# Kernel optimization log

Measured on AMD Instinct MI355X. Metric: run time of the kernel, lower is better.

## Reference

```python
import jax, jax.numpy as jnp
import numpy as np

D_MODEL = 1024
N_HEADS = 16
D_HEAD = 64
LAMBDA_INIT = 0.8  # paper: 0.8 - 0.6*exp(-0.3*(layer-1)); layer=1 -> 0.8


def setup_inputs() -> dict:
    key = jax.random.key(0)
    ks = jax.random.split(key, 6)
    B, S = 2, 2048
    std = 0.02
    x = jax.random.normal(ks[0], (B, S, D_MODEL), dtype=jnp.float32)
    Wq = jax.random.normal(ks[1], (D_MODEL, 2 * N_HEADS * D_HEAD), dtype=jnp.float32) * std
    Wk = jax.random.normal(ks[2], (D_MODEL, 2 * N_HEADS * D_HEAD), dtype=jnp.float32) * std
    Wv = jax.random.normal(ks[3], (D_MODEL, 2 * N_HEADS * D_HEAD), dtype=jnp.float32) * std
    Wo = jax.random.normal(ks[4], (N_HEADS * D_HEAD, D_MODEL), dtype=jnp.float32) * std
    # lambda params initialized to zeros per source (lambda_q1 = zeros(d_head))
    lq1 = jnp.zeros((D_HEAD,), dtype=jnp.float32)
    lk1 = jnp.zeros((D_HEAD,), dtype=jnp.float32)
    lq2 = jnp.zeros((D_HEAD,), dtype=jnp.float32)
    lk2 = jnp.zeros((D_HEAD,), dtype=jnp.float32)
    return {"x": x, "Wq": Wq, "Wk": Wk, "Wv": Wv, "Wo": Wo,
            "lq1": lq1, "lk1": lk1, "lq2": lq2, "lk2": lk2}


def reference(x, Wq, Wk, Wv, Wo, lq1, lk1, lq2, lk2):
    B, S, D = x.shape
    h, dh = N_HEADS, D_HEAD
    # project and split into the two attention-map groups: [B, S, 2, h, dh]
    q = (x @ Wq).reshape(B, S, 2, h, dh)
    k = (x @ Wk).reshape(B, S, 2, h, dh)
    v = (x @ Wv).reshape(B, S, 2, h, dh)
    q1, q2 = q[:, :, 0], q[:, :, 1]  # [B, S, h, dh]
    k1, k2 = k[:, :, 0], k[:, :, 1]
    v1, v2 = v[:, :, 0], v[:, :, 1]

    scale = 1.0 / jnp.sqrt(jnp.asarray(dh, dtype=x.dtype))
    lam = jnp.exp(jnp.dot(lq1, lk1)) - jnp.exp(jnp.dot(lq2, lk2)) + LAMBDA_INIT

    causal = jnp.tril(jnp.ones((S, S), dtype=bool))  # [S, S]
    neg_inf = jnp.asarray(-1e30, dtype=x.dtype)

    s1 = jnp.einsum('bshd,bthd->bhst', q1, k1) * scale
    s2 = jnp.einsum('bshd,bthd->bhst', q2, k2) * scale
    s1 = jnp.where(causal, s1, neg_inf)
    s2 = jnp.where(causal, s2, neg_inf)
    a1 = jax.nn.softmax(s1, axis=-1)
    a2 = jax.nn.softmax(s2, axis=-1)

    # differential attention output per head: A1 @ V1 - lambda * (A2 @ V2)
    o = jnp.einsum('bhst,bthd->bshd', a1, v1) - lam * jnp.einsum('bhst,bthd->bshd', a2, v2)
    o = o.reshape(B, S, h * dh) * (1.0 - LAMBDA_INIT)
    return o @ Wo
```

## Files before the change

### kernel.cpp

```cpp
#include <hip/hip_runtime.h>
#include <hip/hip_bf16.h>

typedef __bf16 bf16_t;
typedef bf16_t bf16x8 __attribute__((ext_vector_type(8)));
typedef float f32x4 __attribute__((ext_vector_type(4)));
typedef float f32x16 __attribute__((ext_vector_type(16)));

static __device__ __forceinline__ f32x4 mfma16(bf16x8 a, bf16x8 b, f32x4 c) {
  return __builtin_amdgcn_mfma_f32_16x16x32_bf16(a, b, c, 0, 0, 0);
}
static __device__ __forceinline__ f32x16 mfma32(bf16x8 a, bf16x8 b, f32x16 c) {
  return __builtin_amdgcn_mfma_f32_32x32x16_bf16(a, b, c, 0, 0, 0);
}

static __device__ __forceinline__ void gload_lds16(const bf16_t* g, bf16_t* l) {
  __builtin_amdgcn_global_load_lds(
      (const __attribute__((address_space(1))) void*)g,
      (__attribute__((address_space(3))) void*)l, 16, 0, 0);
}

static __device__ __forceinline__ unsigned pkbf(float a, float b) {
  union { bf16_t h[2]; unsigned u; } p;
  p.h[0] = (bf16_t)a; p.h[1] = (bf16_t)b;
  return p.u;
}
static __device__ __forceinline__ void pl32swap(unsigned& a, unsigned& b) {
  asm volatile("v_permlane32_swap_b32 %0, %1" : "+v"(a), "+v"(b));
}


__global__ __launch_bounds__(64) void lam_kernel(const float* __restrict__ lq1,
                                                 const float* __restrict__ lk1,
                                                 const float* __restrict__ lq2,
                                                 const float* __restrict__ lk2,
                                                 float* __restrict__ lamp) {
  int l = threadIdx.x;
  float a = lq1[l] * lk1[l];
  float b = lq2[l] * lk2[l];
  #pragma unroll
  for (int msk = 32; msk; msk >>= 1) {
    a += __shfl_xor(a, msk);
    b += __shfl_xor(b, msk);
  }
  if (l == 0) lamp[0] = __expf(a) - __expf(b) + 0.8f;
}

__global__ __launch_bounds__(256) void cvt_x_kernel(const float* __restrict__ x,
                                                    bf16_t* __restrict__ xb) {
  int i = (blockIdx.x * 256 + threadIdx.x) * 4;
  float4 v = *reinterpret_cast<const float4*>(x + i);
  union { bf16_t h[4]; uint2 u; } pk;
  pk.h[0] = (bf16_t)v.x; pk.h[1] = (bf16_t)v.y;
  pk.h[2] = (bf16_t)v.z; pk.h[3] = (bf16_t)v.w;
  *reinterpret_cast<uint2*>(xb + i) = pk.u;
}

__global__ __launch_bounds__(256) void transpose_cvt(const float* __restrict__ W,
                                                     bf16_t* __restrict__ Wt,
                                                     int K, int N) {
  __shared__ float tile[32][33];
  int n0 = blockIdx.x * 32, k0 = blockIdx.y * 32;
  int x = threadIdx.x, y = threadIdx.y;
  #pragma unroll
  for (int i = 0; i < 32; i += 8)
    tile[y + i][x] = W[(size_t)(k0 + y + i) * N + n0 + x];
  __syncthreads();
  #pragma unroll
  for (int i = 0; i < 32; i += 8)
    Wt[(size_t)(n0 + y + i) * K + k0 + x] = (bf16_t)tile[x][y + i];
}

__global__ __launch_bounds__(256) void combine_kernel(const bf16_t* __restrict__ Ob1,
                                                      const bf16_t* __restrict__ Ob2,
                                                      bf16_t* __restrict__ Ob,
                                                      const float* __restrict__ lamp) {
  int i = (blockIdx.x * 256 + threadIdx.x) * 8;
  const float lam = lamp[0];
  bf16x8 a = *reinterpret_cast<const bf16x8*>(Ob1 + i);
  bf16x8 c = *reinterpret_cast<const bf16x8*>(Ob2 + i);
  bf16x8 r;
  #pragma unroll
  for (int j = 0; j < 8; ++j)
    r[j] = (bf16_t)(0.2f * ((float)a[j] - lam * (float)c[j]));
  *reinterpret_cast<bf16x8*>(Ob + i) = r;
}


template <typename OutT>
static __device__ __forceinline__ void gemm_bt_body(const bf16_t* __restrict__ A,
                                                    const bf16_t* __restrict__ Bt,
                                                    OutT* __restrict__ C,
                                                    int M, int N, int K,
                                                    bool vtrans) {
  __shared__ bf16_t As[128 * 32];
  __shared__ bf16_t Bs[128 * 32];
  const int tid = threadIdx.x;
  const int w = tid >> 6, lane = tid & 63;
  const int g = lane >> 4, l15 = lane & 15;
  const int wm = w >> 1, wn = w & 1;

  const int nbx = gridDim.x;
  const int idx = blockIdx.y * nbx + blockIdx.x;
  const int qq = (nbx * gridDim.y) >> 3;
  const int sidx = (idx & 7) * qq + (idx >> 3);
  const int rowBase = (sidx / nbx) * 128, colBase = (sidx % nbx) * 128;

  const int c0 = 2 * w, c1 = 2 * w + 1;
  const int srow0 = 16 * c0 + (lane >> 2);
  const int srow1 = 16 * c1 + (lane >> 2);
  const int scol = (lane & 3) * 8;

  f32x4 acc[4][4] = {};

  for (int k0 = 0; k0 < K; k0 += 32) {
    __syncthreads();
    gload_lds16(A + (size_t)(rowBase + srow0) * K + k0 + scol, &As[c0 * 512]);
    gload_lds16(A + (size_t)(rowBase + srow1) * K + k0 + scol, &As[c1 * 512]);
    gload_lds16(Bt + (size_t)(colBase + srow0) * K + k0 + scol, &Bs[c0 * 512]);
    gload_lds16(Bt + (size_t)(colBase + srow1) * K + k0 + scol, &Bs[c1 * 512]);
    __syncthreads();

    bf16x8 bfr[4];
    #pragma unroll
    for (int j = 0; j < 4; ++j)
      bfr[j] = *reinterpret_cast<const bf16x8*>(&Bs[(wn * 64 + j * 16 + l15) * 32 + g * 8]);
    #pragma unroll
    for (int i = 0; i < 4; ++i) {
      bf16x8 afr = *reinterpret_cast<const bf16x8*>(&As[(wm * 64 + i * 16 + l15) * 32 + g * 8]);
      #pragma unroll
      for (int j = 0; j < 4; ++j)
        acc[i][j] = mfma16(afr, bfr[j], acc[i][j]);
    }
  }

  if (vtrans) {
    #pragma unroll
    for (int i = 0; i < 4; ++i) {
      #pragma unroll
      for (int j = 0; j < 4; ++j) {
        int row = rowBase + wm * 64 + i * 16 + 4 * g;
        int col = colBase + wn * 64 + j * 16 + l15;
        int bb = row >> 11, s = row & 2047;
        union { bf16_t h[4]; uint2 u; } pk;
        #pragma unroll
        for (int r = 0; r < 4; ++r) pk.h[r] = (bf16_t)acc[i][j][r];
        *reinterpret_cast<uint2*>(
            (bf16_t*)C + ((size_t)bb * 2048 + col) * 2048 + s) = pk.u;
      }
    }
  } else {
    #pragma unroll
    for (int i = 0; i < 4; ++i) {
      #pragma unroll
      for (int j = 0; j < 4; ++j) {
        int row = rowBase + wm * 64 + i * 16 + 4 * g;
        int col = colBase + wn * 64 + j * 16 + l15;
        #pragma unroll
        for (int r = 0; r < 4; ++r)
          C[(size_t)(row + r) * N + col] = (OutT)acc[i][j][r];
      }
    }
  }
}

__global__ __launch_bounds__(256) void gemm_qkv(const bf16_t* __restrict__ xb,
                                                const bf16_t* __restrict__ Wqt,
                                                const bf16_t* __restrict__ Wkt,
                                                const bf16_t* __restrict__ Wvt,
                                                bf16_t* __restrict__ Q,
                                                bf16_t* __restrict__ K,
                                                bf16_t* __restrict__ Vtg) {
  const bf16_t* Bt = (blockIdx.z == 0) ? Wqt : (blockIdx.z == 1) ? Wkt : Wvt;
  bf16_t* C = (blockIdx.z == 0) ? Q : (blockIdx.z == 1) ? K : Vtg;
  gemm_bt_body<bf16_t>(xb, Bt, C, 4096, 2048, 1024, blockIdx.z == 2);
}

__global__ __launch_bounds__(256) void gemm_out(const bf16_t* __restrict__ Ob,
                                                const bf16_t* __restrict__ Wot,
                                                float* __restrict__ out) {
  gemm_bt_body<float>(Ob, Wot, out, 4096, 1024, 1024, false);
}


__global__ __launch_bounds__(256, 1)
void attn_kernel(const bf16_t* __restrict__ Qg, const bf16_t* __restrict__ Kg,
                 const bf16_t* __restrict__ Vtg, bf16_t* __restrict__ Ob1,
                 bf16_t* __restrict__ Ob2) {
  __shared__ __align__(16) char ldsbuf[32768];
  __shared__ float lsArr[2][32];

  const int tid = threadIdx.x;
  const int w = tid >> 6, lane = tid & 63;
  const int l31 = lane & 31, hi = lane >> 5;
  const int sw7 = l31 & 7;
  const int rowg = w & 1, keyh = w >> 1;
  const int bx = blockIdx.x;
  const int comp = bx & 1;
  const int rhalf = (bx >> 1) & 1;
  const int bh = (bx >> 2) & 31;
  const int p = bx >> 7;
  const int b = bh >> 4, h = bh & 15;
  const int rowB = b * 2048;
  const float cexp = 0.125f * 1.44269504088896340736f;
  bf16_t* __restrict__ Obc = comp ? Ob2 : Ob1;

  const int lk8 = lane >> 3;
  const int sc8 = (lane & 7) ^ lk8;
  const int lk4 = lane >> 4;
  const int wv = (w - 2) & 1;
  const size_t kOff = (size_t)(rowB + ((w & 1) << 6) + lk8) * 2048 +
                      comp * 1024 + h * 64 + sc8 * 8;
  const size_t vOff = ((size_t)b * 2048 + comp * 1024 + h * 64 +
                       (wv << 5) + lk4) * 2048;

  auto stage = [&](char* bufb, int j0) {
    if (w < 2) {
      const bf16_t* src = Kg + kOff + (size_t)j0 * 2048;
      char* dst = bufb + w * 8192;
      #pragma unroll
      for (int t = 0; t < 8; ++t)
        gload_lds16(src + (size_t)t * (8 * 2048), (bf16_t*)(dst + t * 1024));
    } else {
      const bf16_t* src = Vtg + vOff + j0;
      char* dst = bufb + 16384 + wv * 8192;
      #pragma unroll
      for (int t = 0; t < 8; ++t) {
        int sc16 = (lane & 15) ^ (((t & 1) << 2) + lk4);
        gload_lds16(src + (size_t)t * (4 * 2048) + sc16 * 8,
                    (bf16_t*)(dst + t * 1024));
      }
    }
  };

  f32x16 o[2];
  float ls;
  bf16x8 qf[4];

  auto finalize = [&](int q0, char* scratch) {
    float* sf = (float*)scratch;
    #pragma unroll
    for (int db = 0; db < 2; ++db) {
      __syncthreads();
      if (w >= 2) {
        float* bp = sf + (size_t)((w - 2) * 64 + lane) * 17;
        #pragma unroll
        for (int e = 0; e < 16; ++e) bp[e] = o[db][e];
        if (db == 0) bp[16] = ls;
      }
      __syncthreads();
      if (w < 2) {
        const float* bp = sf + (size_t)(w * 64 + lane) * 17;
        #pragma unroll
        for (int e = 0; e < 16; ++e) o[db][e] += bp[e];
        if (db == 0) ls += bp[16];
      }
    }
    __syncthreads();
    if (w < 2) {
      float tot = ls + __shfl_xor(ls, 32);
      lsArr[w][l31] = 1.f / tot;
    }
    __syncthreads();
    if (w < 2) {
      #pragma unroll
      for (int e = 0; e < 16; ++e) {
        int ql = (e & 3) + 8 * (e >> 2) + 4 * hi;
        float inv = lsArr[w][ql];
        int row = rowB + q0 + rhalf * 64 + w * 32 + ql;
        size_t rb = (size_t)row * 1024 + h * 64 + l31;
        Obc[rb]      = (bf16_t)(o[0][e] * inv);
        Obc[rb + 32] = (bf16_t)(o[1][e] * inv);
      }
    }
  };

  #pragma unroll 1
  for (int i = 0; i <= 16; ++i) {
    const int q0 = (i > p ? 15 - p : p) << 7;
    const int j0 = (i > p ? i - p - 1 : i) << 7;

    __syncthreads();
    stage(ldsbuf, j0);

    if (i == 0 || i == p + 1) {
      #pragma unroll
      for (int s = 0; s < 4; ++s)
        qf[s] = *reinterpret_cast<const bf16x8*>(
            Qg + (size_t)(rowB + q0 + rhalf * 64 + rowg * 32 + l31) * 2048 +
            comp * 1024 + h * 64 + s * 16 + hi * 8);
      o[0] = (f32x16)0.f;
      o[1] = (f32x16)0.f;
      ls = 0.f;
    }

    __syncthreads();

    const char* bufb = (const char*)ldsbuf;
    const int rowbase = q0 + rhalf * 64 + rowg * 32;
    const int qg = rowbase + l31;
    const bool active = (j0 + keyh * 64) <= (rowbase + 31);
    if (active) {
      const bool maskt = (j0 + keyh * 64 + 63) > rowbase;
      const char* Kb = bufb + keyh * 8192;
      const char* Vb = bufb + 16384;
      #pragma unroll
      for (int kb = 0; kb < 2; ++kb) {
        f32x16 sA = {};
        #pragma unroll
        for (int s = 0; s < 4; ++s) {
          int xo = ((2 * s + hi) ^ sw7) << 4;
          bf16x8 kf = *reinterpret_cast<const bf16x8*>(
              Kb + (kb * 32 + l31) * 128 + xo);
          sA = mfma32(kf, qf[s], sA);
        }
        float pv[16];
        #pragma unroll
        for (int e = 0; e < 16; ++e) {
          float v = __builtin_exp2f(sA[e] * cexp);
          if (maskt) {
            int krow = (e & 3) + 8 * (e >> 2) + 4 * hi;
            if (j0 + keyh * 64 + kb * 32 + krow > qg) v = 0.f;
          }
          pv[e] = v;
          ls += v;
        }
        bf16x8 pa[2];
        #pragma unroll
        for (int sp = 0; sp < 2; ++sp) {
          unsigned u0 = pkbf(pv[8 * sp + 0], pv[8 * sp + 1]);
          unsigned u1 = pkbf(pv[8 * sp + 2], pv[8 * sp + 3]);
          unsigned v0 = pkbf(pv[8 * sp + 4], pv[8 * sp + 5]);
          unsigned v1 = pkbf(pv[8 * sp + 6], pv[8 * sp + 7]);
          pl32swap(u0, v0);
          pl32swap(u1, v1);
          union { uint4 u; bf16x8 f; } cvt;
          cvt.u = make_uint4(u0, u1, v0, v1);
          pa[sp] = cvt.f;
        }
        #pragma unroll
        for (int sp = 0; sp < 2; ++sp) {
          int s = kb * 2 + sp;
          int sl = ((keyh * 8) | ((2 * s + hi) ^ sw7)) << 4;
          bf16x8 vf0 = *reinterpret_cast<const bf16x8*>(Vb + l31 * 256 + sl);
          bf16x8 vf1 = *reinterpret_cast<const bf16x8*>(Vb + (32 + l31) * 256 + sl);
          o[0] = mfma32(pa[sp], vf0, o[0]);
          o[1] = mfma32(pa[sp], vf1, o[1]);
        }
      }
    }

    if (i == p || i == 16) finalize(q0, ldsbuf);
  }
}


extern "C" void kernel_launch(void* const* d_in, const int* in_sizes, int n_in,
                              void* d_out, int out_size, void* d_ws, size_t ws_size,
                              hipStream_t stream) {
  const float* x   = (const float*)d_in[0];
  const float* Wq  = (const float*)d_in[1];
  const float* Wk  = (const float*)d_in[2];
  const float* Wv  = (const float*)d_in[3];
  const float* Wo  = (const float*)d_in[4];
  const float* lq1 = (const float*)d_in[5];
  const float* lk1 = (const float*)d_in[6];
  const float* lq2 = (const float*)d_in[7];
  const float* lk2 = (const float*)d_in[8];
  float* out = (float*)d_out;

  char* ws = (char*)d_ws;
  size_t off = 0;
  auto alloc = [&](size_t bytes) -> char* {
    char* p = ws + off;
    off += (bytes + 255) & ~(size_t)255;
    return p;
  };
  bf16_t* xb  = (bf16_t*)alloc((size_t)4096 * 1024 * 2);
  bf16_t* Wqt = (bf16_t*)alloc((size_t)2048 * 1024 * 2);
  bf16_t* Wkt = (bf16_t*)alloc((size_t)2048 * 1024 * 2);
  bf16_t* Wvt = (bf16_t*)alloc((size_t)2048 * 1024 * 2);
  bf16_t* Wot = (bf16_t*)alloc((size_t)1024 * 1024 * 2);
  bf16_t* Qb  = (bf16_t*)alloc((size_t)4096 * 2048 * 2);
  bf16_t* Kb  = (bf16_t*)alloc((size_t)4096 * 2048 * 2);
  bf16_t* Vtg = (bf16_t*)alloc((size_t)4096 * 2048 * 2);
  bf16_t* Ob  = (bf16_t*)alloc((size_t)4096 * 1024 * 2);
  float*  lamp = (float*)alloc(256);

  bf16_t* Ob1 = xb;
  bf16_t* Ob2 = Wqt;

  lam_kernel<<<1, 64, 0, stream>>>(lq1, lk1, lq2, lk2, lamp);
  cvt_x_kernel<<<4096, 256, 0, stream>>>(x, xb);
  transpose_cvt<<<dim3(64, 32), dim3(32, 8), 0, stream>>>(Wq, Wqt, 1024, 2048);
  transpose_cvt<<<dim3(64, 32), dim3(32, 8), 0, stream>>>(Wk, Wkt, 1024, 2048);
  transpose_cvt<<<dim3(64, 32), dim3(32, 8), 0, stream>>>(Wv, Wvt, 1024, 2048);
  transpose_cvt<<<dim3(32, 32), dim3(32, 8), 0, stream>>>(Wo, Wot, 1024, 1024);
  gemm_qkv<<<dim3(16, 32, 3), 256, 0, stream>>>(xb, Wqt, Wkt, Wvt, Qb, Kb, Vtg);
  attn_kernel<<<1024, 256, 0, stream>>>(Qb, Kb, Vtg, Ob1, Ob2);
  combine_kernel<<<2048, 256, 0, stream>>>(Ob1, Ob2, Ob, lamp);
  gemm_out<<<dim3(8, 32), 256, 0, stream>>>(Ob, Wot, out);
}
```

Measured before the change: 216.9 us.

## Use 512-thread attention blocks covering 128 query rows; fold softmax scale into Wq

The attention kernel now launches 512 blocks of 8 waves instead of 1024 blocks of 4 waves. Four waves each cover a 32-row query group, and each block handles all 128 query rows of a tile instead of splitting them into two 64-row halves. This halves the number of times each K/V tile is staged into LDS and merges the split-key reduction into one LDS exchange. The softmax scale and log2(e) factor are folded into Wq during its bf16 conversion, which removes a multiply per score element. Risks: bf16 rounding of Q now includes the scale, and fewer, larger blocks on one CU may change latency hiding.

Result: no change. 216.5 us (-0.2%).

```diff
diff --git a/kernel.cpp b/kernel.cpp
--- a/kernel.cpp
+++ b/kernel.cpp
@@ -57,7 +57,7 @@
 
 __global__ __launch_bounds__(256) void transpose_cvt(const float* __restrict__ W,
                                                      bf16_t* __restrict__ Wt,
-                                                     int K, int N) {
+                                                     int K, int N, float scale) {
   __shared__ float tile[32][33];
   int n0 = blockIdx.x * 32, k0 = blockIdx.y * 32;
   int x = threadIdx.x, y = threadIdx.y;
@@ -67,7 +67,7 @@
   __syncthreads();
   #pragma unroll
   for (int i = 0; i < 32; i += 8)
-    Wt[(size_t)(n0 + y + i) * K + k0 + x] = (bf16_t)tile[x][y + i];
+    Wt[(size_t)(n0 + y + i) * K + k0 + x] = (bf16_t)(tile[x][y + i] * scale);
 }
 
 __global__ __launch_bounds__(256) void combine_kernel(const bf16_t* __restrict__ Ob1,
@@ -182,49 +182,48 @@
 }
 
 
-__global__ __launch_bounds__(256, 1)
+__global__ __launch_bounds__(512, 1)
 void attn_kernel(const bf16_t* __restrict__ Qg, const bf16_t* __restrict__ Kg,
                  const bf16_t* __restrict__ Vtg, bf16_t* __restrict__ Ob1,
                  bf16_t* __restrict__ Ob2) {
   __shared__ __align__(16) char ldsbuf[32768];
-  __shared__ float lsArr[2][32];
+  __shared__ float lsArr[4][32];
+  __shared__ float lsDon[4][64];
 
   const int tid = threadIdx.x;
   const int w = tid >> 6, lane = tid & 63;
   const int l31 = lane & 31, hi = lane >> 5;
   const int sw7 = l31 & 7;
-  const int rowg = w & 1, keyh = w >> 1;
+  const int rowg = w & 3, keyh = w >> 2;
   const int bx = blockIdx.x;
   const int comp = bx & 1;
-  const int rhalf = (bx >> 1) & 1;
-  const int bh = (bx >> 2) & 31;
-  const int p = bx >> 7;
+  const int bh = (bx >> 1) & 31;
+  const int p = bx >> 6;
   const int b = bh >> 4, h = bh & 15;
   const int rowB = b * 2048;
-  const float cexp = 0.125f * 1.44269504088896340736f;
   bf16_t* __restrict__ Obc = comp ? Ob2 : Ob1;
 
   const int lk8 = lane >> 3;
   const int sc8 = (lane & 7) ^ lk8;
   const int lk4 = lane >> 4;
-  const int wv = (w - 2) & 1;
-  const size_t kOff = (size_t)(rowB + ((w & 1) << 6) + lk8) * 2048 +
+  const int wv = (w - 4) & 3;
+  const size_t kOff = (size_t)(rowB + w * 32 + lk8) * 2048 +
                       comp * 1024 + h * 64 + sc8 * 8;
   const size_t vOff = ((size_t)b * 2048 + comp * 1024 + h * 64 +
-                       (wv << 5) + lk4) * 2048;
+                       wv * 16 + lk4) * 2048;
 
   auto stage = [&](char* bufb, int j0) {
-    if (w < 2) {
+    if (w < 4) {
       const bf16_t* src = Kg + kOff + (size_t)j0 * 2048;
-      char* dst = bufb + w * 8192;
-      #pragma unroll
-      for (int t = 0; t < 8; ++t)
+      char* dst = bufb + w * 4096;
+      #pragma unroll
+      for (int t = 0; t < 4; ++t)
         gload_lds16(src + (size_t)t * (8 * 2048), (bf16_t*)(dst + t * 1024));
     } else {
       const bf16_t* src = Vtg + vOff + j0;
-      char* dst = bufb + 16384 + wv * 8192;
-      #pragma unroll
-      for (int t = 0; t < 8; ++t) {
+      char* dst = bufb + 16384 + wv * 4096;
+      #pragma unroll
+      for (int t = 0; t < 4; ++t) {
         int sc16 = (lane & 15) ^ (((t & 1) << 2) + lk4);
         gload_lds16(src + (size_t)t * (4 * 2048) + sc16 * 8,
                     (bf16_t*)(dst + t * 1024));
@@ -236,37 +235,28 @@
   float ls;
   bf16x8 qf[4];
 
-  auto finalize = [&](int q0, char* scratch) {
-    float* sf = (float*)scratch;
-    #pragma unroll
-    for (int db = 0; db < 2; ++db) {
-      __syncthreads();
-      if (w >= 2) {
-        float* bp = sf + (size_t)((w - 2) * 64 + lane) * 17;
-        #pragma unroll
-        for (int e = 0; e < 16; ++e) bp[e] = o[db][e];
-        if (db == 0) bp[16] = ls;
-      }
-      __syncthreads();
-      if (w < 2) {
-        const float* bp = sf + (size_t)(w * 64 + lane) * 17;
-        #pragma unroll
-        for (int e = 0; e < 16; ++e) o[db][e] += bp[e];
-        if (db == 0) ls += bp[16];
-      }
-    }
-    __syncthreads();
-    if (w < 2) {
+  auto finalize = [&](int q0) {
+    float* sf = (float*)ldsbuf;
+    __syncthreads();
+    if (w >= 4) {
+      float* bp = sf + (size_t)((w - 4) * 64 + lane) * 32;
+      #pragma unroll
+      for (int e = 0; e < 16; ++e) { bp[e] = o[0][e]; bp[16 + e] = o[1][e]; }
+      lsDon[w - 4][lane] = ls;
+    }
+    __syncthreads();
+    if (w < 4) {
+      const float* bp = sf + (size_t)(w * 64 + lane) * 32;
+      #pragma unroll
+      for (int e = 0; e < 16; ++e) { o[0][e] += bp[e]; o[1][e] += bp[16 + e]; }
+      ls += lsDon[w][lane];
       float tot = ls + __shfl_xor(ls, 32);
       lsArr[w][l31] = 1.f / tot;
-    }
-    __syncthreads();
-    if (w < 2) {
       #pragma unroll
       for (int e = 0; e < 16; ++e) {
         int ql = (e & 3) + 8 * (e >> 2) + 4 * hi;
         float inv = lsArr[w][ql];
-        int row = rowB + q0 + rhalf * 64 + w * 32 + ql;
+        int row = rowB + q0 + w * 32 + ql;
         size_t rb = (size_t)row * 1024 + h * 64 + l31;
         Obc[rb]      = (bf16_t)(o[0][e] * inv);
         Obc[rb + 32] = (bf16_t)(o[1][e] * inv);
@@ -286,8 +276,8 @@
       #pragma unroll
       for (int s = 0; s < 4; ++s)
         qf[s] = *reinterpret_cast<const bf16x8*>(
-            Qg + (size_t)(rowB + q0 + rhalf * 64 + rowg * 32 + l31) * 2048 +
-            comp * 1024 + h * 64 + s * 16 + hi * 8);
+            Qg + (size_t)(rowB + q0 + rowg * 32 + l31) * 2048 + comp * 1024 +
+            h * 64 + s * 16 + hi * 8);
       o[0] = (f32x16)0.f;
       o[1] = (f32x16)0.f;
       ls = 0.f;
@@ -296,7 +286,7 @@
     __syncthreads();
 
     const char* bufb = (const char*)ldsbuf;
-    const int rowbase = q0 + rhalf * 64 + rowg * 32;
+    const int rowbase = q0 + rowg * 32;
     const int qg = rowbase + l31;
     const bool active = (j0 + keyh * 64) <= (rowbase + 31);
     if (active) {
@@ -316,7 +306,7 @@
         float pv[16];
         #pragma unroll
         for (int e = 0; e < 16; ++e) {
-          float v = __builtin_exp2f(sA[e] * cexp);
+          float v = __builtin_exp2f(sA[e]);
           if (maskt) {
             int krow = (e & 3) + 8 * (e >> 2) + 4 * hi;
             if (j0 + keyh * 64 + kb * 32 + krow > qg) v = 0.f;
@@ -349,7 +339,7 @@
       }
     }
 
-    if (i == p || i == 16) finalize(q0, ldsbuf);
+    if (i == p || i == 16) finalize(q0);
   }
 }
 
@@ -389,14 +379,16 @@
   bf16_t* Ob1 = xb;
   bf16_t* Ob2 = Wqt;
 
+  const float QSCALE = 0.125f * 1.44269504088896340736f;
+
   lam_kernel<<<1, 64, 0, stream>>>(lq1, lk1, lq2, lk2, lamp);
   cvt_x_kernel<<<4096, 256, 0, stream>>>(x, xb);
-  transpose_cvt<<<dim3(64, 32), dim3(32, 8), 0, stream>>>(Wq, Wqt, 1024, 2048);
-  transpose_cvt<<<dim3(64, 32), dim3(32, 8), 0, stream>>>(Wk, Wkt, 1024, 2048);
-  transpose_cvt<<<dim3(64, 32), dim3(32, 8), 0, stream>>>(Wv, Wvt, 1024, 2048);
-  transpose_cvt<<<dim3(32, 32), dim3(32, 8), 0, stream>>>(Wo, Wot, 1024, 1024);
+  transpose_cvt<<<dim3(64, 32), dim3(32, 8), 0, stream>>>(Wq, Wqt, 1024, 2048, QSCALE);
+  transpose_cvt<<<dim3(64, 32), dim3(32, 8), 0, stream>>>(Wk, Wkt, 1024, 2048, 1.0f);
+  transpose_cvt<<<dim3(64, 32), dim3(32, 8), 0, stream>>>(Wv, Wvt, 1024, 2048, 1.0f);
+  transpose_cvt<<<dim3(32, 32), dim3(32, 8), 0, stream>>>(Wo, Wot, 1024, 1024, 1.0f);
   gemm_qkv<<<dim3(16, 32, 3), 256, 0, stream>>>(xb, Wqt, Wkt, Wvt, Qb, Kb, Vtg);
-  attn_kernel<<<1024, 256, 0, stream>>>(Qb, Kb, Vtg, Ob1, Ob2);
+  attn_kernel<<<512, 512, 0, stream>>>(Qb, Kb, Vtg, Ob1, Ob2);
   combine_kernel<<<2048, 256, 0, stream>>>(Ob1, Ob2, Ob, lamp);
   gemm_out<<<dim3(8, 32), 256, 0, stream>>>(Ob, Wot, out);
 }
```
